# Kernel tuning notes

Measured on AMD Instinct MI355X. Metric: run time of the kernel, lower is better.

The kernel has to match this reference:

```python
import jax, jax.numpy as jnp
import numpy as np
import math

DIM = 1024
SEQ = 4096
BATCH = 4
CHUNK = 64
LN_EPS = 1e-5


def setup_inputs() -> dict:
    key = jax.random.key(0)
    ks = jax.random.split(key, 16)
    d = DIM
    def lin(k):
        k1, k2 = jax.random.split(k)
        lim = 1.0 / math.sqrt(d)
        W = jax.random.uniform(k1, (d, d), jnp.float32, -lim, lim)
        b = jax.random.uniform(k2, (d,), jnp.float32, -lim, lim)
        return W, b
    Wk, bk = lin(ks[0])
    Wv, bv = lin(ks[1])
    Wq, bq = lin(ks[2])
    Wkm, bkm = lin(ks[3])
    Wqm, bqm = lin(ks[4])
    Wo, bo = lin(ks[5])
    return {
        "x": jax.random.normal(ks[6], (BATCH, SEQ, d), jnp.float32),
        "base_phases": jax.random.normal(ks[7], (SEQ, d), jnp.float32) * math.pi,
        "Wk": Wk, "bk": bk, "Wv": Wv, "bv": bv, "Wq": Wq, "bq": bq,
        "Wkm": Wkm, "bkm": bkm, "Wqm": Wqm, "bqm": bqm,
        "mod_scale": jnp.ones((1,), jnp.float32) * 0.1,
        "ln_g": jnp.ones((d,), jnp.float32),
        "ln_b": jnp.zeros((d,), jnp.float32),
        "Wo": Wo, "bo": bo,
    }


def reference(x, base_phases, Wk, bk, Wv, bv, Wq, bq, Wkm, bkm, Wqm, bqm,
              mod_scale, ln_g, ln_b, Wo, bo):
    B, S, D = x.shape
    key = x @ Wk + bk
    value = x @ Wv + bv
    query = x @ Wq + bq
    base = base_phases[:S][None]                      # [1,S,D]
    key_phase = base + (key @ Wkm + bkm) * mod_scale   # [B,S,D]
    query_phase = base + (query @ Wqm + bqm) * mod_scale
    bound_real = value * jnp.cos(key_phase)
    bound_imag = value * jnp.sin(key_phase)
    pad = (CHUNK - S % CHUNK) % CHUNK
    if pad > 0:
        pcfg = ((0, 0), (0, pad), (0, 0))
        bound_real = jnp.pad(bound_real, pcfg)
        bound_imag = jnp.pad(bound_imag, pcfg)
        query_phase = jnp.pad(query_phase, pcfg)
    P = S + pad
    nc = P // CHUNK
    br = bound_real.reshape(B, nc, CHUNK, D)
    bi = bound_imag.reshape(B, nc, CHUNK, D)
    qp = query_phase.reshape(B, nc, CHUNK, D)
    mem_real = jnp.cumsum(br, axis=2)
    mem_imag = jnp.cumsum(bi, axis=2)
    retrieved = mem_real * jnp.cos(qp) + mem_imag * jnp.sin(qp)
    retrieved = retrieved.reshape(B, P, D)[:, :S] / math.sqrt(D)
    mu = jnp.mean(retrieved, axis=-1, keepdims=True)
    var = jnp.mean(jnp.square(retrieved - mu), axis=-1, keepdims=True)
    normed = (retrieved - mu) * jax.lax.rsqrt(var + LN_EPS) * ln_g + ln_b
    out = normed @ Wo + bo
    return x + out
```

## Files before the change

### kernel.cpp

```cpp
#include <hip/hip_runtime.h>

#define DIM 1024
#define SEQ 4096
#define MROWS 16384
#define CHUNK 64
#define NCHUNKBLKS 256

typedef float  f32x4  __attribute__((ext_vector_type(4)));
typedef __bf16 bf16x8 __attribute__((ext_vector_type(8)));
typedef __bf16 bf16x4 __attribute__((ext_vector_type(4)));

__device__ __forceinline__ void gld16(const void* g, void* l) {
  __builtin_amdgcn_global_load_lds((__attribute__((address_space(1))) void*)g,
                                   (__attribute__((address_space(3))) void*)l,
                                   16, 0, 0);
}

__device__ __forceinline__ f32x4 ld4f(const __bf16* p) {
  bf16x4 v = *(const bf16x4*)p;
  f32x4 r;
#pragma unroll
  for (int j = 0; j < 4; ++j) r[j] = (float)v[j];
  return r;
}

#define KLOOP64(As_, Bs_, Ag_, Bg_, AsL_, BsL_)                                  \
  for (int kt = 0; kt < DIM / 64; ++kt) {                                        \
    const __bf16* a_ = Ag_ + kt * 64;                                            \
    const __bf16* b_ = Bg_ + kt * 64;                                            \
    _Pragma("unroll") for (int i = 0; i < 4; ++i) {                              \
      gld16(a_ + i * 32 * DIM, AsL_ + i * 4096);                                 \
      gld16(b_ + i * 32 * DIM, BsL_ + i * 4096);                                 \
    }                                                                            \
    __syncthreads();                                                             \
    const bf16x8* Av_ = (const bf16x8*)(As_);                                    \
    const bf16x8* Bv_ = (const bf16x8*)(Bs_);                                    \
    _Pragma("unroll") for (int kk = 0; kk < 2; ++kk) {                           \
      bf16x8 af[4], bfv[4];                                                      \
      const int pc = (kk * 4 + kg) ^ (lane & 7);                                 \
      _Pragma("unroll") for (int i = 0; i < 4; ++i) af[i]  = Av_[(ar + i*16)*8 + pc]; \
      _Pragma("unroll") for (int i = 0; i < 4; ++i) bfv[i] = Bv_[(br + i*16)*8 + pc]; \
      _Pragma("unroll") for (int mi = 0; mi < 4; ++mi)                           \
        _Pragma("unroll") for (int ni = 0; ni < 4; ++ni)                         \
          acc[mi][ni] = __builtin_amdgcn_mfma_f32_16x16x32_bf16(af[mi], bfv[ni], acc[mi][ni], 0, 0, 0); \
    }                                                                            \
    __syncthreads();                                                             \
  }

#define GEMM_PROLOG64(A_, B_)                                                    \
  const int tid  = threadIdx.x;                                                  \
  const int lane = tid & 63;                                                     \
  const int widx = tid >> 6;                                                     \
  const int wr   = widx >> 1, wc = widx & 1;                                     \
  const int kc = ((lane & 7) ^ ((lane >> 3) & 7)) * 8;                           \
  const __bf16* Ag = (A_) + (size_t)(row0 + widx * 8 + (lane >> 3)) * DIM + kc;  \
  const __bf16* Bg = (B_) + (size_t)(col0 + widx * 8 + (lane >> 3)) * DIM + kc;  \
  char* AsL = (char*)As + widx * 1024;                                           \
  char* BsL = (char*)Bs + widx * 1024;                                           \
  f32x4 acc[4][4] = {};                                                          \
  const int ar = wr * 64 + (lane & 15);                                          \
  const int br = wc * 64 + (lane & 15);                                          \
  const int kg = lane >> 4;

template <int MODE, int SWZ>
__global__ __launch_bounds__(256, 2)
void gemm_bt(const __bf16* __restrict__ A, const __bf16* __restrict__ Bt,
             const float* __restrict__ bias, void* __restrict__ outp,
             const float* __restrict__ mscp, const float* __restrict__ xres,
             const __bf16* __restrict__ A2, const __bf16* __restrict__ Bt2,
             void* __restrict__ out2)
{
  __shared__ __bf16 As[128 * 64];
  __shared__ __bf16 Bs[128 * 64];
  if (MODE == 5 && blockIdx.z == 1) { A = A2; Bt = Bt2; outp = out2; }

  int row_t, col_t;
  if (SWZ == 1) {
    const int b = blockIdx.y * 8 + blockIdx.x;
    const int xcd = b & 7, slot = b >> 3;
    col_t = slot & 7;
    row_t = (xcd << 4) | (slot >> 3);
  } else {
    row_t = blockIdx.y; col_t = blockIdx.x;
  }
  const int row0 = row_t * 128, col0 = col_t * 128;

  GEMM_PROLOG64(A, Bt)
  KLOOP64(As, Bs, Ag, Bg, AsL, BsL)

  const int ccol = col0 + wc * 64 + (lane & 15);
  const int crow = row0 + wr * 64 + kg * 4;
  float bvv[4];
  if (MODE != 5) {
#pragma unroll
    for (int ni = 0; ni < 4; ++ni) bvv[ni] = bias[ccol + ni * 16];
  }
  float ms = 0.f;
  if (MODE == 5) ms = mscp[0];
#pragma unroll
  for (int mi = 0; mi < 4; ++mi)
#pragma unroll
    for (int ni = 0; ni < 4; ++ni)
#pragma unroll
      for (int r = 0; r < 4; ++r) {
        const int row = crow + mi * 16 + r;
        const int col = ccol + ni * 16;
        const size_t idx = (size_t)row * DIM + col;
        if (MODE == 3) {
          ((float*)outp)[idx] = acc[mi][ni][r] + bvv[ni] + xres[idx];
        } else {
          ((__bf16*)outp)[idx] = (__bf16)(acc[mi][ni][r] * ms);
        }
      }
}

__global__ __launch_bounds__(256, 2)
void gemm3(const __bf16* __restrict__ A, const __bf16* __restrict__ Ball,
           const float* __restrict__ biasAll,
           __bf16* __restrict__ valb, __bf16* __restrict__ kphb,
           __bf16* __restrict__ qphb)
{
  __shared__ __bf16 As[128 * 64];
  __shared__ __bf16 Bs[128 * 64];
  const int b = blockIdx.y * 24 + blockIdx.x;
  const int xcd = b & 7, p = b >> 3;
  const int col_t = p % 24;
  const int row_t = (xcd << 4) + p / 24;
  const int row0 = row_t * 128, col0 = col_t * 128;

  GEMM_PROLOG64(A, Ball)
  KLOOP64(As, Bs, Ag, Bg, AsL, BsL)

  const int band = col_t >> 3;
  const int ccol = col0 + wc * 64 + (lane & 15);
  const int lcol0 = ccol & 1023;
  const int crow = row0 + wr * 64 + kg * 4;
  float bvv[4];
#pragma unroll
  for (int ni = 0; ni < 4; ++ni) bvv[ni] = biasAll[ccol + ni * 16];
  __bf16* outb = (band == 0) ? valb : (band == 1) ? kphb : qphb;
#pragma unroll
  for (int mi = 0; mi < 4; ++mi)
#pragma unroll
    for (int ni = 0; ni < 4; ++ni)
#pragma unroll
      for (int r = 0; r < 4; ++r) {
        const int row = crow + mi * 16 + r;
        const size_t idx = (size_t)row * DIM + lcol0 + ni * 16;
        outb[idx] = (__bf16)(acc[mi][ni][r] + bvv[ni]);
      }
}

__global__ __launch_bounds__(256)
void phasor_ln(const __bf16* __restrict__ val, const __bf16* __restrict__ kph,
               const __bf16* __restrict__ qph, const __bf16* __restrict__ baseb,
               const float* __restrict__ g, const float* __restrict__ lb,
               __bf16* __restrict__ nb)
{
  const int t = threadIdx.x;
  const size_t r0 = (size_t)blockIdx.x * CHUNK;
  const int c = t * 4;
  const f32x4 gv  = ((const f32x4*)g)[t];
  const f32x4 lbv = ((const f32x4*)lb)[t];
  __shared__ float red[8];
  float mr[4] = {0.f, 0.f, 0.f, 0.f};
  float mi[4] = {0.f, 0.f, 0.f, 0.f};
  size_t base = r0 * DIM + c;
  f32x4 v  = ld4f(val + base);
  f32x4 kp = ld4f(kph + base);
  f32x4 qp = ld4f(qph + base);
  f32x4 bp = ld4f(baseb + (size_t)((r0) & (SEQ - 1)) * DIM + c);
  for (int r = 0; r < CHUNK; ++r) {
    const size_t nbase = base + ((r + 1 < CHUNK) ? DIM : 0);
    const int nrow = (int)((r0 + ((r + 1 < CHUNK) ? r + 1 : r)) & (SEQ - 1));
    f32x4 nv  = ld4f(val + nbase);
    f32x4 nkp = ld4f(kph + nbase);
    f32x4 nqp = ld4f(qph + nbase);
    f32x4 nbp = ld4f(baseb + (size_t)nrow * DIM + c);
    float ret[4];
    float s = 0.f, q = 0.f;
#pragma unroll
    for (int j = 0; j < 4; ++j) {
      float sk, ck, sq, cq;
      __sincosf(bp[j] + kp[j], &sk, &ck);
      mr[j] += v[j] * ck;
      mi[j] += v[j] * sk;
      __sincosf(bp[j] + qp[j], &sq, &cq);
      ret[j] = (mr[j] * cq + mi[j] * sq) * 0.03125f;
      s += ret[j];
      q += ret[j] * ret[j];
    }
#pragma unroll
    for (int off = 32; off > 0; off >>= 1) {
      s += __shfl_down(s, off);
      q += __shfl_down(q, off);
    }
    if ((t & 63) == 0) { red[t >> 6] = s; red[4 + (t >> 6)] = q; }
    __syncthreads();
    const float mu   = (red[0] + red[1] + red[2] + red[3]) * (1.0f / DIM);
    const float varr = (red[4] + red[5] + red[6] + red[7]) * (1.0f / DIM) - mu * mu;
    const float rinv = rsqrtf(varr + 1e-5f);
    bf16x4 o;
#pragma unroll
    for (int j = 0; j < 4; ++j) o[j] = (__bf16)((ret[j] - mu) * rinv * gv[j] + lbv[j]);
    *(bf16x4*)(nb + base) = o;
    __syncthreads();
    base += DIM;
    v = nv; kp = nkp; qp = nqp; bp = nbp;
  }
}

__global__ void f2b_kernel(const float* __restrict__ in, __bf16* __restrict__ out, int n4) {
  int i = blockIdx.x * 256 + threadIdx.x;
  if (i >= n4) return;
  f32x4 vv = ((const f32x4*)in)[i];
  bf16x4 o;
#pragma unroll
  for (int j = 0; j < 4; ++j) o[j] = (__bf16)vv[j];
  ((bf16x4*)out)[i] = o;
}

__global__ void wrapb_kernel(const float* __restrict__ in, __bf16* __restrict__ out, int n4) {
  int i = blockIdx.x * 256 + threadIdx.x;
  if (i >= n4) return;
  f32x4 vv = ((const f32x4*)in)[i];
  bf16x4 o;
#pragma unroll
  for (int j = 0; j < 4; ++j) {
    float v = vv[j];
    v -= 6.2831853f * rintf(v * 0.15915494f);
    o[j] = (__bf16)v;
  }
  ((bf16x4*)out)[i] = o;
}

__global__ void f2b2_kernel(const float* __restrict__ i0, __bf16* __restrict__ o0,
                            const float* __restrict__ i1, __bf16* __restrict__ o1, int n4) {
  int i = blockIdx.x * 256 + threadIdx.x;
  if (i >= n4) return;
  const float* in = blockIdx.y ? i1 : i0;
  __bf16* out = blockIdx.y ? o1 : o0;
  f32x4 vv = ((const f32x4*)in)[i];
  bf16x4 o;
#pragma unroll
  for (int j = 0; j < 4; ++j) o[j] = (__bf16)vv[j];
  ((bf16x4*)out)[i] = o;
}

__global__ void transpose_f2b4(const float* __restrict__ s0, __bf16* __restrict__ d0,
                               const float* __restrict__ s1, __bf16* __restrict__ d1,
                               const float* __restrict__ s2, __bf16* __restrict__ d2,
                               const float* __restrict__ s3, __bf16* __restrict__ d3) {
  __shared__ float tle[32][33];
  const float* W; __bf16* Wt;
  switch (blockIdx.z) {
    case 0: W = s0; Wt = d0; break;
    case 1: W = s1; Wt = d1; break;
    case 2: W = s2; Wt = d2; break;
    default: W = s3; Wt = d3; break;
  }
  const int tx = threadIdx.x, ty = threadIdx.y;
  const int bx = blockIdx.x * 32, by = blockIdx.y * 32;
  for (int i = ty; i < 32; i += 8) tle[i][tx] = W[(size_t)(by + i) * DIM + bx + tx];
  __syncthreads();
  for (int i = ty; i < 32; i += 8) Wt[(size_t)(bx + i) * DIM + by + tx] = (__bf16)tle[tx][i];
}

__global__ void biascomb3(const float* __restrict__ bk, const float* __restrict__ Wkm,
                          const float* __restrict__ bkm, const float* __restrict__ bq,
                          const float* __restrict__ Wqm, const float* __restrict__ bqm,
                          const float* __restrict__ bv, const float* __restrict__ ms,
                          float* __restrict__ biasAll)
{
  const int n = blockIdx.x * 256 + threadIdx.x;
  const int which = blockIdx.y;
  if (which == 2) { biasAll[n] = bv[n]; return; }
  const float* bs = which ? bq : bk;
  const float* W  = which ? Wqm : Wkm;
  const float* ba = which ? bqm : bkm;
  float s = 0.f;
  for (int k = 0; k < DIM; ++k) s += bs[k] * W[(size_t)k * DIM + n];
  biasAll[1024 + which * 1024 + n] = (s + ba[n]) * ms[0];
}

__global__ void copyx_kernel(const float* __restrict__ x, float* __restrict__ out, int n4) {
  int i = blockIdx.x * 256 + threadIdx.x;
  if (i >= n4) return;
  ((f32x4*)out)[i] = ((const f32x4*)x)[i];
}

extern "C" void kernel_launch(void* const* d_in, const int* in_sizes, int n_in,
                              void* d_out, int out_size, void* d_ws, size_t ws_size,
                              hipStream_t stream)
{
  (void)in_sizes; (void)n_in; (void)out_size;
  const float* x     = (const float*)d_in[0];
  const float* basep = (const float*)d_in[1];
  const float* Wk    = (const float*)d_in[2];
  const float* bk    = (const float*)d_in[3];
  const float* Wv    = (const float*)d_in[4];
  const float* bv    = (const float*)d_in[5];
  const float* Wq    = (const float*)d_in[6];
  const float* bq    = (const float*)d_in[7];
  const float* Wkm   = (const float*)d_in[8];
  const float* bkm   = (const float*)d_in[9];
  const float* Wqm   = (const float*)d_in[10];
  const float* bqm   = (const float*)d_in[11];
  const float* msc   = (const float*)d_in[12];
  const float* lng   = (const float*)d_in[13];
  const float* lnb   = (const float*)d_in[14];
  const float* Wo    = (const float*)d_in[15];
  const float* bo    = (const float*)d_in[16];

  char* ws = (char*)d_ws;
  const size_t MB = 1ull << 20;
  if (ws_size < 153 * MB) {
    copyx_kernel<<<MROWS * DIM / 4 / 256, 256, 0, stream>>>(x, (float*)d_out, MROWS * DIM / 4);
    return;
  }

  __bf16* xb     = (__bf16*)ws;
  __bf16* valb   = (__bf16*)(ws +  32 * MB);
  __bf16* kphb   = (__bf16*)(ws +  64 * MB);
  __bf16* qphb   = (__bf16*)(ws +  96 * MB);
  __bf16* Ball   = (__bf16*)(ws + 128 * MB);
  __bf16* WoT    = (__bf16*)(ws + 134 * MB);
  __bf16* TWkm   = (__bf16*)(ws + 136 * MB);
  __bf16* BWk    = (__bf16*)(ws + 138 * MB);
  __bf16* TWqm   = (__bf16*)(ws + 140 * MB);
  __bf16* BWq    = (__bf16*)(ws + 142 * MB);
  __bf16* baseb  = (__bf16*)(ws + 144 * MB);
  float*  biasAll= (float*)(ws + 152 * MB);
  __bf16* nbuf   = xb;

  f2b_kernel<<<MROWS * DIM / 4 / 256, 256, 0, stream>>>(x, xb, MROWS * DIM / 4);
  wrapb_kernel<<<SEQ * DIM / 4 / 256, 256, 0, stream>>>(basep, baseb, SEQ * DIM / 4);
  dim3 tg(32, 32, 4), tb(32, 8);
  transpose_f2b4<<<tg, tb, 0, stream>>>(Wv, Ball, Wo, WoT, Wkm, TWkm, Wqm, TWqm);
  f2b2_kernel<<<dim3(DIM * DIM / 4 / 256, 2), 256, 0, stream>>>(Wk, BWk, Wq, BWq, DIM * DIM / 4);
  gemm_bt<5, 0><<<dim3(8, 8, 2), 256, 0, stream>>>(
      TWkm, BWk, nullptr, Ball + (size_t)1024 * DIM, msc, nullptr,
      TWqm, BWq, Ball + (size_t)2048 * DIM);
  biascomb3<<<dim3(4, 3), 256, 0, stream>>>(bk, Wkm, bkm, bq, Wqm, bqm, bv, msc, biasAll);

  gemm3<<<dim3(24, 128), 256, 0, stream>>>(xb, Ball, biasAll, valb, kphb, qphb);
  phasor_ln<<<NCHUNKBLKS, 256, 0, stream>>>(valb, kphb, qphb, baseb, lng, lnb, nbuf);
  gemm_bt<3, 1><<<dim3(8, 128), 256, 0, stream>>>(
      nbuf, WoT, bo, d_out, nullptr, x, nullptr, nullptr, nullptr);
}
```

Measured before the change: 288.9 us.

## Batch LN reductions in phasor kernel, split bias GEMV, remap gemm3 tiles

The phasor/LayerNorm kernel now processes 8 rows per barrier pair, batching the shuffle reductions and cutting the __syncthreads count per chunk by a factor of 8. The cost is more registers and the loss of the explicit next-row prefetch. The bias-combination GEMV is split into an init kernel plus a K-split kernel using vectorized loads and atomicAdd, so it runs with more parallelism than the old 12-block serial loop. gemm3 block-to-tile mapping is reordered so consecutive blocks on an XCD walk rows within a column tile, changing L2 reuse of B versus A.

```diff
diff --git a/kernel.cpp b/kernel.cpp
--- a/kernel.cpp
+++ b/kernel.cpp
@@ -124,8 +124,8 @@
   __shared__ __bf16 Bs[128 * 64];
   const int b = blockIdx.y * 24 + blockIdx.x;
   const int xcd = b & 7, p = b >> 3;
-  const int col_t = p % 24;
-  const int row_t = (xcd << 4) + p / 24;
+  const int col_t = p / 16;
+  const int row_t = (xcd << 4) + (p & 15);
   const int row0 = row_t * 128, col0 = col_t * 128;
 
   GEMM_PROLOG64(A, Ball)
@@ -158,55 +158,60 @@
                __bf16* __restrict__ nb)
 {
   const int t = threadIdx.x;
+  const int w = t >> 6, lane = t & 63;
   const size_t r0 = (size_t)blockIdx.x * CHUNK;
   const int c = t * 4;
   const f32x4 gv  = ((const f32x4*)g)[t];
   const f32x4 lbv = ((const f32x4*)lb)[t];
-  __shared__ float red[8];
+  __shared__ float redS[8][4], redQ[8][4];
   float mr[4] = {0.f, 0.f, 0.f, 0.f};
   float mi[4] = {0.f, 0.f, 0.f, 0.f};
-  size_t base = r0 * DIM + c;
-  f32x4 v  = ld4f(val + base);
-  f32x4 kp = ld4f(kph + base);
-  f32x4 qp = ld4f(qph + base);
-  f32x4 bp = ld4f(baseb + (size_t)((r0) & (SEQ - 1)) * DIM + c);
-  for (int r = 0; r < CHUNK; ++r) {
-    const size_t nbase = base + ((r + 1 < CHUNK) ? DIM : 0);
-    const int nrow = (int)((r0 + ((r + 1 < CHUNK) ? r + 1 : r)) & (SEQ - 1));
-    f32x4 nv  = ld4f(val + nbase);
-    f32x4 nkp = ld4f(kph + nbase);
-    f32x4 nqp = ld4f(qph + nbase);
-    f32x4 nbp = ld4f(baseb + (size_t)nrow * DIM + c);
-    float ret[4];
-    float s = 0.f, q = 0.f;
-#pragma unroll
-    for (int j = 0; j < 4; ++j) {
-      float sk, ck, sq, cq;
-      __sincosf(bp[j] + kp[j], &sk, &ck);
-      mr[j] += v[j] * ck;
-      mi[j] += v[j] * sk;
-      __sincosf(bp[j] + qp[j], &sq, &cq);
-      ret[j] = (mr[j] * cq + mi[j] * sq) * 0.03125f;
-      s += ret[j];
-      q += ret[j] * ret[j];
+  for (int rb = 0; rb < 8; ++rb) {
+    float ret[8][4], ss[8], qq[8];
+#pragma unroll
+    for (int r = 0; r < 8; ++r) {
+      const int row = rb * 8 + r;
+      const size_t base = (r0 + row) * DIM + c;
+      const f32x4 v  = ld4f(val + base);
+      const f32x4 kp = ld4f(kph + base);
+      const f32x4 qp = ld4f(qph + base);
+      const f32x4 bp = ld4f(baseb + (size_t)((r0 + row) & (SEQ - 1)) * DIM + c);
+      float s = 0.f, q = 0.f;
+#pragma unroll
+      for (int j = 0; j < 4; ++j) {
+        float sk, ck, sq, cq;
+        __sincosf(bp[j] + kp[j], &sk, &ck);
+        mr[j] += v[j] * ck;
+        mi[j] += v[j] * sk;
+        __sincosf(bp[j] + qp[j], &sq, &cq);
+        ret[r][j] = (mr[j] * cq + mi[j] * sq) * 0.03125f;
+        s += ret[r][j];
+        q += ret[r][j] * ret[r][j];
+      }
+      ss[r] = s; qq[r] = q;
     }
 #pragma unroll
-    for (int off = 32; off > 0; off >>= 1) {
-      s += __shfl_down(s, off);
-      q += __shfl_down(q, off);
+    for (int off = 32; off > 0; off >>= 1)
+#pragma unroll
+      for (int r = 0; r < 8; ++r) {
+        ss[r] += __shfl_down(ss[r], off);
+        qq[r] += __shfl_down(qq[r], off);
+      }
+    if (lane == 0)
+#pragma unroll
+      for (int r = 0; r < 8; ++r) { redS[r][w] = ss[r]; redQ[r][w] = qq[r]; }
+    __syncthreads();
+#pragma unroll
+    for (int r = 0; r < 8; ++r) {
+      const float mu   = (redS[r][0] + redS[r][1] + redS[r][2] + redS[r][3]) * (1.0f / DIM);
+      const float varr = (redQ[r][0] + redQ[r][1] + redQ[r][2] + redQ[r][3]) * (1.0f / DIM) - mu * mu;
+      const float rinv = rsqrtf(varr + 1e-5f);
+      bf16x4 o;
+#pragma unroll
+      for (int j = 0; j < 4; ++j) o[j] = (__bf16)((ret[r][j] - mu) * rinv * gv[j] + lbv[j]);
+      *(bf16x4*)(nb + (r0 + rb * 8 + r) * DIM + c) = o;
     }
-    if ((t & 63) == 0) { red[t >> 6] = s; red[4 + (t >> 6)] = q; }
     __syncthreads();
-    const float mu   = (red[0] + red[1] + red[2] + red[3]) * (1.0f / DIM);
-    const float varr = (red[4] + red[5] + red[6] + red[7]) * (1.0f / DIM) - mu * mu;
-    const float rinv = rsqrtf(varr + 1e-5f);
-    bf16x4 o;
-#pragma unroll
-    for (int j = 0; j < 4; ++j) o[j] = (__bf16)((ret[j] - mu) * rinv * gv[j] + lbv[j]);
-    *(bf16x4*)(nb + base) = o;
-    __syncthreads();
-    base += DIM;
-    v = nv; kp = nkp; qp = nqp; bp = nbp;
   }
 }
 
@@ -266,21 +271,37 @@
   for (int i = ty; i < 32; i += 8) Wt[(size_t)(bx + i) * DIM + by + tx] = (__bf16)tle[tx][i];
 }
 
-__global__ void biascomb3(const float* __restrict__ bk, const float* __restrict__ Wkm,
-                          const float* __restrict__ bkm, const float* __restrict__ bq,
-                          const float* __restrict__ Wqm, const float* __restrict__ bqm,
-                          const float* __restrict__ bv, const float* __restrict__ ms,
-                          float* __restrict__ biasAll)
-{
+__global__ void biasinit(const float* __restrict__ bv, const float* __restrict__ bkm,
+                         const float* __restrict__ bqm, const float* __restrict__ ms,
+                         float* __restrict__ biasAll) {
   const int n = blockIdx.x * 256 + threadIdx.x;
+  const float m = ms[0];
+  biasAll[n] = bv[n];
+  biasAll[1024 + n] = bkm[n] * m;
+  biasAll[2048 + n] = bqm[n] * m;
+}
+
+__global__ void biasacc(const float* __restrict__ bk, const float* __restrict__ Wkm,
+                        const float* __restrict__ bq, const float* __restrict__ Wqm,
+                        const float* __restrict__ ms, float* __restrict__ biasAll) {
+  const int t = threadIdx.x;
   const int which = blockIdx.y;
-  if (which == 2) { biasAll[n] = bv[n]; return; }
+  const int k0 = blockIdx.z * 128;
   const float* bs = which ? bq : bk;
   const float* W  = which ? Wqm : Wkm;
-  const float* ba = which ? bqm : bkm;
-  float s = 0.f;
-  for (int k = 0; k < DIM; ++k) s += bs[k] * W[(size_t)k * DIM + n];
-  biasAll[1024 + which * 1024 + n] = (s + ba[n]) * ms[0];
+  const int n0 = t * 4;
+  float s0 = 0.f, s1 = 0.f, s2 = 0.f, s3 = 0.f;
+  for (int k = k0; k < k0 + 128; ++k) {
+    const float b = bs[k];
+    const f32x4 wv = *(const f32x4*)(W + (size_t)k * DIM + n0);
+    s0 += b * wv[0]; s1 += b * wv[1]; s2 += b * wv[2]; s3 += b * wv[3];
+  }
+  const float m = ms[0];
+  float* dst = biasAll + 1024 + which * 1024 + n0;
+  atomicAdd(dst + 0, s0 * m);
+  atomicAdd(dst + 1, s1 * m);
+  atomicAdd(dst + 2, s2 * m);
+  atomicAdd(dst + 3, s3 * m);
 }
 
 __global__ void copyx_kernel(const float* __restrict__ x, float* __restrict__ out, int n4) {
@@ -341,7 +362,8 @@
   gemm_bt<5, 0><<<dim3(8, 8, 2), 256, 0, stream>>>(
       TWkm, BWk, nullptr, Ball + (size_t)1024 * DIM, msc, nullptr,
       TWqm, BWq, Ball + (size_t)2048 * DIM);
-  biascomb3<<<dim3(4, 3), 256, 0, stream>>>(bk, Wkm, bkm, bq, Wqm, bqm, bv, msc, biasAll);
+  biasinit<<<4, 256, 0, stream>>>(bv, bkm, bqm, msc, biasAll);
+  biasacc<<<dim3(1, 2, 8), 256, 0, stream>>>(bk, Wkm, bq, Wqm, msc, biasAll);
 
   gemm3<<<dim3(24, 128), 256, 0, stream>>>(xb, Ball, biasAll, valb, kphb, qphb);
   phasor_ln<<<NCHUNKBLKS, 256, 0, stream>>>(valb, kphb, qphb, baseb, lng, lnb, nbuf);
```

After: 264.9 us. 1.09x faster.
